# Kernel tuning notes

Hardware: AMD Instinct MI355X
Metric: run time of the kernel (lower is better)

The kernel has to match this reference:

```python
import jax, jax.numpy as jnp
import numpy as np

B, N, DY, STD, T = 2, 8000, 12, 6, 30
DX = 0.5
DYG = 0.5
DT = 1.0

def _mlp(x, params):
    n = len(params)
    for i, (W, b) in enumerate(params):
        x = x @ W + b
        if i < n - 1:
            x = jax.nn.relu(x)
    return x

def _process_param(D, mu, coeff_vec):
    ds = DY // 3
    d33 = ds * ds
    m33 = [coeff_vec[i * d33:(i + 1) * d33].reshape(ds, ds) for i in range(4)]
    base = 4 * d33
    dd = ds * ds - ds
    diag = []
    for i in range(3):
        aij = coeff_vec[base + i * dd:base + (i + 1) * dd].reshape(ds - 1, ds)
        m = jnp.concatenate([jnp.ones((ds - 1, 1), aij.dtype), aij], axis=1).reshape(-1)
        m = jnp.concatenate([m, jnp.ones((1,), aij.dtype)]).reshape(ds, ds)
        diag.append(m)
    z = jnp.zeros((ds, ds), coeff_vec.dtype)
    rows = jnp.concatenate([
        jnp.concatenate([diag[0], z, m33[0]], axis=1),
        jnp.concatenate([z, diag[1], m33[1]], axis=1),
        jnp.concatenate([m33[2], m33[3], diag[2]], axis=1)], axis=0)
    coeffM = jax.nn.relu(rows)  # [DY, DY]
    ds0 = jnp.zeros((ds,), D.dtype)
    Dij = jax.nn.relu(jnp.concatenate([ds0, D]))  # [DY]
    MUij = jax.nn.relu(jnp.concatenate([mu[:ds], ds0, mu[-ds:]]))  # [DY]
    return coeffM, Dij, MUij

def _overlap(t, g):
    # overlap length of unit intervals centered at t and g
    omin = jax.nn.relu((t - 0.5) - (g - 0.5)) + (g - 0.5)
    omax = (t + 0.5) - jax.nn.relu((t + 0.5) - (g + 0.5))
    return jax.nn.relu(omax - omin)

def _trans_probs(dx_, dy_):
    gx, gy = jnp.meshgrid(jnp.arange(5.0), jnp.arange(5.0), indexing='ij')
    grid = jnp.stack([gx, gy], -1).reshape(25, 2)
    xl = _overlap(dx_[..., None, :], grid[:, 1].reshape(1, 1, 25, 1))
    yl = _overlap(dy_[..., None, :], grid[:, 0].reshape(1, 1, 25, 1))
    return xl * yl  # [B,N,25,C]

def _aggre(inp, a0):
    x = inp[:, a0]  # [B,N,25,C] gather
    w = jnp.concatenate([jnp.ones((1,)), jnp.full((24,), 0.01)]).reshape(1, 1, 25, 1)
    return jnp.concatenate([inp, (x * w).sum(-2)], axis=-1)

def _pde(phi, feat_dy, feat_st, D, mu, coeff_vec, trans_p, q_p, dec_p, adj4, adj25, ckpt=False):
    a4 = adj4[0]   # [N,4]
    a0 = adj25[0]  # [N,25]
    coeffM, Dij, MUij = _process_param(D, mu, coeff_vec)
    phie = phi[..., None]
    pn = phie[:, a4]  # [B,N,4,1]
    gpx = (pn[:, :, 1] - pn[:, :, 0]) / (2 * DX)
    gpy = (pn[:, :, 3] - pn[:, :, 2]) / (2 * DYG)
    phi_ag = _aggre(phie, a0)      # constant across steps
    st_ag = _aggre(feat_st, a0)    # constant across steps
    D_bn = jnp.broadcast_to(jax.lax.stop_gradient(Dij), (B, N, DY))
    MU_bn = jnp.broadcast_to(jax.lax.stop_gradient(MUij), (B, N, DY))

    def step(feat, _):
        last = feat
        fn = feat[:, a4]  # [B,N,4,C]
        J = (fn[:, :, 0] + fn[:, :, 1] - 2 * feat) / DX ** 2 + (fn[:, :, 2] + fn[:, :, 3] - 2 * feat) / DYG ** 2
        fxn = (gpx * feat)[:, a4]
        fyn = (gpy * feat)[:, a4]
        Fdiv = (fxn[:, :, 1] - fxn[:, :, 0]) / (2 * DX) + (fyn[:, :, 3] - fyn[:, :, 2]) / (2 * DYG)
        u_diff = jnp.einsum('bnc,cd->bnd', Dij * J - MUij * Fdiv, coeffM)
        mass = jnp.where(last == 0, 1.0, last)
        a_x = jnp.clip(jnp.einsum('bnc,cd->bnd', MUij * gpx, coeffM) / mass, -2.0, 2.0)
        a_y = jnp.clip(jnp.einsum('bnc,cd->bnd', MUij * gpy, coeffM) / mass, -2.0, 2.0)
        probs = _trans_probs(a_x * DT, a_y * DT)  # [B,N,25,C]
        src = probs * last[:, :, None, :]
        scat = lambda idx, s: jnp.zeros((N, DY), s.dtype).at[idx.reshape(-1)].add(s.reshape(-1, DY))
        u_rig = jax.vmap(scat)(adj25, src) - last  # scatter_add over nodes then sum over 25
        feat_tr = jnp.concatenate([_aggre(feat, a0), phi_ag, D_bn, MU_bn, st_ag], -1)  # [B,N,62]
        mix = jax.nn.sigmoid(_mlp(feat_tr, trans_p)[..., -1:])
        delta_u = mix * u_diff + (1 - mix) * u_rig
        feat_q = jnp.concatenate([_aggre(last, a0), phi_ag, st_ag], -1)  # [B,N,38]
        q0 = _mlp(feat_q, q_p)
        new = last + delta_u + q0
        fu = _mlp(jnp.concatenate([new, feat_st], -1), dec_p)  # [B,N,1]
        return new, (fu[..., 0], mix[..., 0], q0, new)

    body = jax.checkpoint(step) if ckpt else step
    _, (us_s, mix_s, q0_s, fd_s) = jax.lax.scan(body, feat_dy, None, length=T)
    us = jnp.moveaxis(us_s, 0, -1).reshape(B, N, 1, T)
    mix_m = jnp.moveaxis(mix_s, 0, -1).reshape(B, N, 1, T)
    q0_m = jnp.moveaxis(q0_s, 0, -1).reshape(B, N, DY, 1, T)
    fd = jnp.moveaxis(fd_s, 0, 2).reshape(B, N, 1, T, DY)
    return us, mix_m, q0_m, fd

def setup_inputs():
    key = jax.random.key(0)
    ks = jax.random.split(key, 24)
    def lin(k, i, o):
        kw, kb = jax.random.split(k)
        return (0.1 * jax.random.normal(kw, (i, o), jnp.float32),
                0.01 * jax.random.normal(kb, (o,), jnp.float32))
    tp = [lin(ks[0], 62, 64), lin(ks[1], 64, 32), lin(ks[2], 32, 26)]
    qp = [lin(ks[3], 38, 64), lin(ks[4], 64, 32), lin(ks[5], 32, 12)]
    dp = [lin(ks[6], 18, 32), lin(ks[7], 32, 32), lin(ks[8], 32, 64), lin(ks[9], 64, 1)]
    inp = {
        'phi': jax.random.normal(ks[10], (B, N), jnp.float32),
        'feat_dy': jax.random.uniform(ks[11], (B, N, DY), jnp.float32),
        'feat_st': jax.random.normal(ks[12], (B, N, STD), jnp.float32),
        'D': jnp.ones((2 * (DY // 3),), jnp.float32) * 0.05,
        'mu': jnp.ones((2 * (DY // 3),), jnp.float32) * 0.05,
        'coeff_vec': jnp.ones((DY * DY - 2 * (DY // 3) ** 2 - DY,), jnp.float32) * 0.05,
        'adj4': jax.random.randint(ks[13], (B, N, 4), 0, N),
        'adj25': jax.random.randint(ks[14], (B, N, 25), 0, N),
    }
    for name, p in [('trans', tp), ('q', qp), ('dec', dp)]:
        for i, (W, b) in enumerate(p):
            inp[name + '_W' + str(i)] = W
            inp[name + '_b' + str(i)] = b
    return inp

def reference(phi, feat_dy, feat_st, D, mu, coeff_vec,
              trans_W0, trans_b0, trans_W1, trans_b1, trans_W2, trans_b2,
              q_W0, q_b0, q_W1, q_b1, q_W2, q_b2,
              dec_W0, dec_b0, dec_W1, dec_b1, dec_W2, dec_b2, dec_W3, dec_b3,
              adj4, adj25):
    trans_p = [(trans_W0, trans_b0), (trans_W1, trans_b1), (trans_W2, trans_b2)]
    q_p = [(q_W0, q_b0), (q_W1, q_b1), (q_W2, q_b2)]
    dec_p = [(dec_W0, dec_b0), (dec_W1, dec_b1), (dec_W2, dec_b2), (dec_W3, dec_b3)]
    return _pde(phi, feat_dy, feat_st, D, mu, coeff_vec, trans_p, q_p, dec_p, adj4, adj25)
```

## Files before the change

### kernel.cpp

```cpp
#include <hip/hip_runtime.h>
#include <hip/hip_fp16.h>
#include <math.h>


namespace {
constexpr int NB = 2;
constexpr int NN = 8000;
constexpr int BN = NB * NN;
constexpr int TS = 30;
constexpr int CAP = 64;

constexpr int P_T0 = 0;
constexpr int P_Q0 = 1536;
constexpr int P_W1 = 3072;
constexpr int P_Q2 = 7168;
constexpr int P_Z  = 7552;
constexpr int P_D0 = 7584;
constexpr int P_D1 = 7968;
constexpr int P_D2 = 8992;
constexpr int P_D3 = 11040;
constexpr int P_BT1 = 11104;
constexpr int P_BQ1 = 11136;
constexpr int P_BQ2 = 11168;
constexpr int P_BD1 = 11184;
constexpr int P_BD2 = 11216;
constexpr int P_MISC= 11280;
constexpr int PACK_N = 11296;

constexpr int A_AG = 0;
constexpr int A_NV = 0;
constexpr int A_H1 = 24;
constexpr int A_D1 = 24;
constexpr int A_D2 = 56;
constexpr int A_H2 = 152;
constexpr int A_SLOT = 216;

constexpr int O_COEFF = 0;
constexpr int O_CFT   = 144;
constexpr int O_DIJ   = 288;
constexpr int O_MUIJ  = 300;
constexpr int O_MC    = 312;
constexpr int O_PACK  = 336;
constexpr int O_GPX   = O_PACK + PACK_N + 16;
constexpr int O_GPY   = O_GPX + BN;
constexpr int O_H1T   = O_GPY + BN;
constexpr int O_H1Q   = O_H1T + BN*64;
constexpr int O_H1D   = O_H1Q + BN*64;
constexpr int O_FEATA = O_H1D + BN*32;
constexpr int O_FEATB = O_FEATA + BN*12;
constexpr int O_AXY2A = O_FEATB + BN*12;
constexpr int O_AXY2B = O_AXY2A + BN*24;
constexpr int O_ACT   = O_AXY2B + BN*24;
constexpr int O_FLTEND= O_ACT + BN*48;
constexpr int O_STG   = O_FLTEND + BN + BN*CAP;
constexpr int STG_N = TS*BN*12;
constexpr size_t WS_NEED = (size_t)(O_STG + STG_N) * 4;

constexpr int OUS  = 0;
constexpr int OMIX = BN*TS;
constexpr int OQ0  = 2*BN*TS;
constexpr int OFD  = OQ0 + BN*12*TS;
}

__device__ __forceinline__ float group5_sum(float v, int lane) {
  int g = lane / 12, c = lane % 12;
  float s1 = __shfl(v, c + 12*((g+1)%5));
  float s2 = __shfl(v, c + 12*((g+2)%5));
  float s3 = __shfl(v, c + 12*((g+3)%5));
  float s4 = __shfl(v, c + 12*((g+4)%5));
  return v + s1 + s2 + s3 + s4;
}

__device__ __forceinline__ float pack_axy(float a, float b) {
  union { __half2 h2; float f; } cv;
  cv.h2 = __floats2half2_rn(a, b);
  return cv.f;
}
__device__ __forceinline__ void unpack_axy(float p, float& a, float& b) {
  union { float f; __half2 h2; } cv;
  cv.f = p;
  a = __low2float(cv.h2);
  b = __high2float(cv.h2);
}

__global__ void k_setup_small(const float* __restrict__ D, const float* __restrict__ mu,
                              const float* __restrict__ cv, float* ws) {
  int t = threadIdx.x;
  for (int e = t; e < 144; e += 256) {
    int r = e / 12, q = e % 12;
    int rb = r >> 2, cb = q >> 2, ri = r & 3, qi = q & 3;
    float val = 0.f;
    if (rb == cb) {
      int f = ri*4 + qi;
      if (f % 5 == 0) val = 1.f;
      else val = cv[64 + rb*12 + (f/5)*4 + (f%5) - 1];
    } else if (rb == 0 && cb == 2) val = cv[     ri*4 + qi];
    else if   (rb == 1 && cb == 2) val = cv[16 + ri*4 + qi];
    else if   (rb == 2 && cb == 0) val = cv[32 + ri*4 + qi];
    else if   (rb == 2 && cb == 1) val = cv[48 + ri*4 + qi];
    ws[O_COEFF + e] = fmaxf(val, 0.f);
  }
  if (t < 12) {
    ws[O_DIJ + t]  = (t < 4) ? 0.f : fmaxf(D[t-4], 0.f);
    ws[O_MUIJ + t] = (t < 4) ? fmaxf(mu[t], 0.f) : ((t < 8) ? 0.f : fmaxf(mu[t-4], 0.f));
  }
  __syncthreads();
  if (t < 144) {
    int r = t / 12, c = t % 12;
    ws[O_CFT + c*12 + r] = ws[O_COEFF + t];
  }
  if (t < 12) {
    float acc = 0.f;
    for (int c = 0; c < 12; c++) acc += ws[O_MUIJ + c] * ws[O_COEFF + c*12 + t];
    ws[O_MC + t] = acc;
  }
}

__global__ void k_xpose(const float* __restrict__ Wt0, const float* __restrict__ Wq0,
                        const float* __restrict__ Wt1, const float* __restrict__ Wq1,
                        const float* __restrict__ Wt2, const float* __restrict__ Wq2,
                        const float* __restrict__ Wd0, const float* __restrict__ Wd1,
                        const float* __restrict__ Wd2, const float* __restrict__ Wd3,
                        const float* __restrict__ bt1, const float* __restrict__ bq1,
                        const float* __restrict__ bt2, const float* __restrict__ bq2,
                        const float* __restrict__ bd1, const float* __restrict__ bd2,
                        const float* __restrict__ bd3,
                        float* ws) {
  const int t = blockIdx.x * blockDim.x + threadIdx.x;
  const int G = gridDim.x * blockDim.x;
  float* P = ws + O_PACK;
  for (int e = t; e < 1536; e += G) {
    int q = e / 256, r = e % 256, l = r / 4, j = r % 4;
    P[P_T0 + e] = Wt0[(4*q+j)*64 + l];
    P[P_Q0 + e] = Wq0[(4*q+j)*64 + l];
  }
  for (int e = t; e < 4096; e += G) {
    int q = e / 256, r = e % 256, l = r / 4, j = r % 4;
    P[P_W1 + e] = (l < 32) ? Wt1[(4*q+j)*32 + l] : Wq1[(4*q+j)*32 + (l-32)];
  }
  for (int e = t; e < 384; e += G) {
    int q = e / 48, r = e % 48, c = r / 4, j = r % 4;
    P[P_Q2 + e] = Wq2[(4*q+j)*12 + c];
  }
  for (int e = t; e < 32; e += G) P[P_Z + e] = Wt2[e*26 + 25];
  for (int e = t; e < 384; e += G) {
    int q = e / 128, r = e % 128, l = r / 4, j = r % 4;
    P[P_D0 + e] = Wd0[(4*q+j)*32 + l];
  }
  for (int e = t; e < 1024; e += G) {
    int q = e / 128, r = e % 128, l = r / 4, j = r % 4;
    P[P_D1 + e] = Wd1[(4*q+j)*32 + l];
  }
  for (int e = t; e < 2048; e += G) {
    int q = e / 256, r = e % 256, l = r / 4, j = r % 4;
    P[P_D2 + e] = Wd2[(4*q+j)*64 + l];
  }
  for (int e = t; e < 64; e += G) P[P_D3 + e] = Wd3[e];
  for (int e = t; e < 32; e += G) {
    P[P_BT1 + e] = bt1[e];
    P[P_BQ1 + e] = bq1[e];
    P[P_BD1 + e] = bd1[e];
  }
  for (int e = t; e < 12; e += G) P[P_BQ2 + e] = bq2[e];
  for (int e = t; e < 64; e += G) P[P_BD2 + e] = bd2[e];
  if (t == 0) { P[P_MISC + 0] = bd3[0]; P[P_MISC + 1] = bt2[25]; }
}

__global__ __launch_bounds__(256) void k_setup_node(
    const float* __restrict__ phi, const float* __restrict__ feat_dy,
    const float* __restrict__ feat_st,
    const int* __restrict__ adj4, const int* __restrict__ adj25,
    const float* __restrict__ Wt0, const float* __restrict__ bt0,
    const float* __restrict__ Wq0, const float* __restrict__ bq0,
    const float* __restrict__ Wd0, const float* __restrict__ bd0,
    float* ws, int* wsi) {
  const int wid  = (blockIdx.x * blockDim.x + threadIdx.x) >> 6;
  const int lane = threadIdx.x & 63;
  if (wid >= BN) return;
  const int b = wid / NN, n = wid % NN;

  const int* a4 = adj4 + n*4;
  const float gpx = phi[b*NN + a4[1]] - phi[b*NN + a4[0]];
  const float gpy = phi[b*NN + a4[3]] - phi[b*NN + a4[2]];
  if (lane == 0) { ws[O_GPX + wid] = gpx; ws[O_GPY + wid] = gpy; wsi[wid] = 0; }

  int idx = 0; float w = 0.f;
  if (lane < 25) { idx = adj25[n*25 + lane]; w = (lane == 0) ? 1.f : 0.01f; }
  float phiw = (lane < 25) ? w * phi[b*NN + idx] : 0.f;
  #pragma unroll
  for (int s = 32; s > 0; s >>= 1) phiw += __shfl_xor(phiw, s);

  float stv[6], stw[6];
  #pragma unroll
  for (int j = 0; j < 6; j++) {
    float x = (lane < 25) ? w * feat_st[(b*NN + idx)*6 + j] : 0.f;
    #pragma unroll
    for (int s = 32; s > 0; s >>= 1) x += __shfl_xor(x, s);
    stw[j] = x;
    stv[j] = feat_st[(b*NN + n)*6 + j];
  }
  const float phiv = phi[b*NN + n];

  float hT = bt0[lane] + phiv*Wt0[24*64 + lane] + phiw*Wt0[25*64 + lane];
  float hQ = bq0[lane] + phiv*Wq0[24*64 + lane] + phiw*Wq0[25*64 + lane];
  #pragma unroll
  for (int i = 0; i < 12; i++) {
    hT = fmaf(ws[O_DIJ  + i], Wt0[(26+i)*64 + lane], hT);
    hT = fmaf(ws[O_MUIJ + i], Wt0[(38+i)*64 + lane], hT);
  }
  #pragma unroll
  for (int j = 0; j < 6; j++) {
    hT = fmaf(stv[j], Wt0[(50+j)*64 + lane], hT);
    hT = fmaf(stw[j], Wt0[(56+j)*64 + lane], hT);
    hQ = fmaf(stv[j], Wq0[(26+j)*64 + lane], hQ);
    hQ = fmaf(stw[j], Wq0[(32+j)*64 + lane], hQ);
  }
  ws[O_H1T + wid*64 + lane] = hT;
  ws[O_H1Q + wid*64 + lane] = hQ;
  if (lane < 32) {
    float hD = bd0[lane];
    #pragma unroll
    for (int j = 0; j < 6; j++) hD = fmaf(stv[j], Wd0[(12+j)*32 + lane], hD);
    ws[O_H1D + wid*32 + lane] = hD;
  }
  if (lane < 12) {
    float f = feat_dy[wid*12 + lane];
    ws[O_FEATA + wid*12 + lane] = f;
    float mass = (f == 0.f) ? 1.f : f;
    float mc = ws[O_MC + lane];
    float axv = fminf(fmaxf(gpx*mc/mass, -2.f), 2.f);
    float ayv = fminf(fmaxf(gpy*mc/mass, -2.f), 2.f);
    float2* a2a = (float2*)(ws + O_AXY2A);
    a2a[wid*12 + lane] = make_float2(f, pack_axy(axv, ayv));
  }
}

__global__ void k_build_rev(const int* __restrict__ adj25, int* wsi) {
  int i = blockIdx.x * blockDim.x + threadIdx.x;
  if (i >= BN * 25) return;
  int b = i / (NN * 25);
  int rem = i % (NN * 25);
  int m = rem / 25, k = rem % 25;
  int tgt = adj25[i];
  int slot = atomicAdd(&wsi[b*NN + tgt], 1);
  if (slot < CAP) wsi[BN + (b*NN + tgt)*CAP + slot] = (m << 5) | k;
}

__global__ __launch_bounds__(512) void k_gather(
    const float* __restrict__ ws,
    const int* __restrict__ rcnt, const int* __restrict__ rent,
    const float* __restrict__ fsrc, const float2* __restrict__ a2src,
    const int* __restrict__ adj4, const int* __restrict__ adj25,
    float* __restrict__ actb) {
  const int wid_raw = (int)((blockIdx.x * blockDim.x + threadIdx.x) >> 6);
  if (wid_raw >= BN) return;
  const int wid  = __builtin_amdgcn_readfirstlane(wid_raw);
  const int lane = threadIdx.x & 63;
  const int c12  = lane % 12;
  const int g    = lane / 12;
  const int b = wid / NN, n = wid % NN;

  const int* a4p = adj4 + n*4;
  const int m0 = a4p[0], m1 = a4p[1], m2 = a4p[2], m3 = a4p[3];
  int cnt = rcnt[wid]; if (cnt > CAP) cnt = CAP;
  const int idxv = (lane < 25) ? adj25[n*25 + lane] : 0;
  const int pkv  = rent[wid*CAP + lane];
  const float f_c  = fsrc[wid*12 + c12];
  const float dij  = ws[O_DIJ  + c12];
  const float muij = ws[O_MUIJ + c12];
  const float4* CFTp = (const float4*)(ws + O_CFT + c12*12);
  const float4 cf0 = CFTp[0], cf1 = CFTp[1], cf2 = CFTp[2];

  float agw = 0.f;
  {
    const int i0 = __shfl(idxv, g);
    const int i1 = __shfl(idxv, g + 5);
    const int i2 = __shfl(idxv, g + 10);
    const int i3 = __shfl(idxv, g + 15);
    const int i4 = __shfl(idxv, g + 20);
    if (g < 5) {
      const float v0 = fsrc[(b*NN + i0)*12 + c12];
      const float v1 = fsrc[(b*NN + i1)*12 + c12];
      const float v2 = fsrc[(b*NN + i2)*12 + c12];
      const float v3 = fsrc[(b*NN + i3)*12 + c12];
      const float v4 = fsrc[(b*NN + i4)*12 + c12];
      const float w0 = (g == 0) ? 1.f : 0.01f;
      agw = fmaf(w0,    v0, agw);
      agw = fmaf(0.01f, v1, agw);
      agw = fmaf(0.01f, v2, agw);
      agw = fmaf(0.01f, v3, agw);
      agw = fmaf(0.01f, v4, agw);
    }
    agw = group5_sum(agw, lane);
  }

  float udiff;
  {
    const float f0 = fsrc[(b*NN+m0)*12 + c12];
    const float f1 = fsrc[(b*NN+m1)*12 + c12];
    const float f2 = fsrc[(b*NN+m2)*12 + c12];
    const float f3 = fsrc[(b*NN+m3)*12 + c12];
    const float gx0 = ws[O_GPX + b*NN + m0], gx1 = ws[O_GPX + b*NN + m1];
    const float gy2 = ws[O_GPY + b*NN + m2], gy3 = ws[O_GPY + b*NN + m3];
    const float J = 4.f * ((f0+f1+f2+f3) - 4.f*f_c);
    const float Fdiv = gx1*f1 - gx0*f0 + gy3*f3 - gy2*f2;
    const float v = dij*J - muij*Fdiv;
    float acc;
    acc  = __shfl(v, 0) * cf0.x;
    acc  = fmaf(__shfl(v, 1), cf0.y, acc);
    acc  = fmaf(__shfl(v, 2), cf0.z, acc);
    acc  = fmaf(__shfl(v, 3), cf0.w, acc);
    acc  = fmaf(__shfl(v, 4), cf1.x, acc);
    acc  = fmaf(__shfl(v, 5), cf1.y, acc);
    acc  = fmaf(__shfl(v, 6), cf1.z, acc);
    acc  = fmaf(__shfl(v, 7), cf1.w, acc);
    acc  = fmaf(__shfl(v, 8), cf2.x, acc);
    acc  = fmaf(__shfl(v, 9), cf2.y, acc);
    acc  = fmaf(__shfl(v,10), cf2.z, acc);
    acc  = fmaf(__shfl(v,11), cf2.w, acc);
    udiff = acc;
  }

  float urig;
  {
    float usc = 0.f;
    #pragma unroll
    for (int it = 0; it < 8; ++it) {
      const int e = g + 5*it;
      const bool val = (g < 5) && (e < cnt);
      const int pk = __shfl(pkv, e & 63);
      const int m = pk >> 5, k = pk & 31;
      const int off = val ? ((b*NN + m)*12 + c12) : (wid*12 + c12);
      const float2 sm = a2src[off];
      float ax, ay; unpack_axy(sm.y, ax, ay);
      const float kx = (float)(k - (k/5)*5);
      const float ky = (float)(k/5);
      const float px = fmaxf(1.f - fabsf(ax - kx), 0.f);
      const float py = fmaxf(1.f - fabsf(ay - ky), 0.f);
      usc = fmaf(val ? px*py : 0.f, sm.x, usc);
    }
    if (cnt > 40) {
      #pragma unroll
      for (int it = 8; it < 13; ++it) {
        const int e = g + 5*it;
        const bool val = (g < 5) && (e < cnt);
        const int pk = __shfl(pkv, e & 63);
        const int m = pk >> 5, k = pk & 31;
        const int off = val ? ((b*NN + m)*12 + c12) : (wid*12 + c12);
        const float2 sm = a2src[off];
        float ax, ay; unpack_axy(sm.y, ax, ay);
        const float kx = (float)(k - (k/5)*5);
        const float ky = (float)(k/5);
        const float px = fmaxf(1.f - fabsf(ax - kx), 0.f);
        const float py = fmaxf(1.f - fabsf(ay - ky), 0.f);
        usc = fmaf(val ? px*py : 0.f, sm.x, usc);
      }
    }
    usc = group5_sum(usc, lane);
    urig = usc - f_c;
  }

  const float ov = (lane < 12) ? agw : ((lane < 24) ? udiff : urig);
  if (lane < 36) actb[wid*48 + lane] = ov;
}

__global__ __launch_bounds__(512) void k_mlp(
    const float* __restrict__ ws, const float* __restrict__ actb, int t,
    const float* __restrict__ fsrc,
    float* __restrict__ fdst, float2* __restrict__ a2dst,
    float* __restrict__ stg, int use_stage,
    float* __restrict__ out) {
  __shared__ __attribute__((aligned(16))) float sh[PACK_N + 16*A_SLOT];
  const int tid = threadIdx.x;
  {
    const float4* wp = (const float4*)(ws + O_PACK);
    float4* sp = (float4*)sh;
    for (int e = tid; e < PACK_N/4; e += 512) sp[e] = wp[e];
  }
  __syncthreads();

  const int wv   = tid >> 6;
  const int wvq  = __builtin_amdgcn_readfirstlane(wv);
  const int lane = tid & 63;
  const int c12 = lane % 12;
  const int l32 = lane & 31;
  const bool isQ = lane >= 32;
  float* act0 = sh + PACK_N + (wvq*2 + 0)*A_SLOT;
  float* act1 = sh + PACK_N + (wvq*2 + 1)*A_SLOT;

  const float mcv = ws[O_MC + c12];

  #pragma unroll 1
  for (int pass = 0; pass < 2; pass++) {
    const int nb = (blockIdx.x*16 + pass*8 + wvq) * 2;

    float f_c[2], udiff[2], urig[2];
    #pragma unroll
    for (int j = 0; j < 2; j++) {
      const int wid = nb + j;
      float* actj = j ? act1 : act0;
      f_c[j] = fsrc[wid*12 + c12];
      const float agv = actb[wid*48 + c12];
      udiff[j] = actb[wid*48 + 12 + c12];
      urig[j]  = actb[wid*48 + 24 + c12];
      if (lane < 24) actj[A_AG + lane] = (lane < 12) ? f_c[j] : agv;
    }

    {
      float h1t0 = ws[O_H1T + nb*64 + lane];
      float h1q0 = ws[O_H1Q + nb*64 + lane];
      float h1t1 = ws[O_H1T + (nb+1)*64 + lane];
      float h1q1 = ws[O_H1Q + (nb+1)*64 + lane];
      #pragma unroll
      for (int q = 0; q < 6; q++) {
        const float4 wt = *(const float4*)&sh[P_T0 + q*256 + lane*4];
        const float4 wq = *(const float4*)&sh[P_Q0 + q*256 + lane*4];
        const float4 a0 = *(const float4*)&act0[A_AG + 4*q];
        const float4 a1 = *(const float4*)&act1[A_AG + 4*q];
        h1t0 = fmaf(a0.x, wt.x, h1t0); h1q0 = fmaf(a0.x, wq.x, h1q0);
        h1t0 = fmaf(a0.y, wt.y, h1t0); h1q0 = fmaf(a0.y, wq.y, h1q0);
        h1t0 = fmaf(a0.z, wt.z, h1t0); h1q0 = fmaf(a0.z, wq.z, h1q0);
        h1t0 = fmaf(a0.w, wt.w, h1t0); h1q0 = fmaf(a0.w, wq.w, h1q0);
        h1t1 = fmaf(a1.x, wt.x, h1t1); h1q1 = fmaf(a1.x, wq.x, h1q1);
        h1t1 = fmaf(a1.y, wt.y, h1t1); h1q1 = fmaf(a1.y, wq.y, h1q1);
        h1t1 = fmaf(a1.z, wt.z, h1t1); h1q1 = fmaf(a1.z, wq.z, h1q1);
        h1t1 = fmaf(a1.w, wt.w, h1t1); h1q1 = fmaf(a1.w, wq.w, h1q1);
      }
      act0[A_H1 + lane]      = fmaxf(h1t0, 0.f);
      act0[A_H1 + 64 + lane] = fmaxf(h1q0, 0.f);
      act1[A_H1 + lane]      = fmaxf(h1t1, 0.f);
      act1[A_H1 + 64 + lane] = fmaxf(h1q1, 0.f);
    }

    {
      const int hoff = isQ ? 64 : 0;
      float h2_0 = isQ ? sh[P_BQ1 + l32] : sh[P_BT1 + l32];
      float h2_1 = h2_0;
      #pragma unroll
      for (int q = 0; q < 16; q++) {
        const float4 w  = *(const float4*)&sh[P_W1 + q*256 + lane*4];
        const float4 a0 = *(const float4*)&act0[A_H1 + hoff + 4*q];
        const float4 a1 = *(const float4*)&act1[A_H1 + hoff + 4*q];
        h2_0 = fmaf(a0.x, w.x, h2_0); h2_1 = fmaf(a1.x, w.x, h2_1);
        h2_0 = fmaf(a0.y, w.y, h2_0); h2_1 = fmaf(a1.y, w.y, h2_1);
        h2_0 = fmaf(a0.z, w.z, h2_0); h2_1 = fmaf(a1.z, w.z, h2_1);
        h2_0 = fmaf(a0.w, w.w, h2_0); h2_1 = fmaf(a1.w, w.w, h2_1);
      }
      act0[A_H2 + lane] = fmaxf(h2_0, 0.f);
      act1[A_H2 + lane] = fmaxf(h2_1, 0.f);
    }

    float mix[2], q0v[2];
    {
      float mz0 = sh[P_MISC + 1], mz1 = mz0;
      float q00 = sh[P_BQ2 + c12], q01 = q00;
      #pragma unroll
      for (int q = 0; q < 8; q++) {
        const float4 wz  = *(const float4*)&sh[P_Z + 4*q];
        const float4 wq  = *(const float4*)&sh[P_Q2 + q*48 + c12*4];
        const float4 at0 = *(const float4*)&act0[A_H2 + 4*q];
        const float4 aq0 = *(const float4*)&act0[A_H2 + 32 + 4*q];
        const float4 at1 = *(const float4*)&act1[A_H2 + 4*q];
        const float4 aq1 = *(const float4*)&act1[A_H2 + 32 + 4*q];
        mz0 = fmaf(at0.x, wz.x, mz0); q00 = fmaf(aq0.x, wq.x, q00);
        mz0 = fmaf(at0.y, wz.y, mz0); q00 = fmaf(aq0.y, wq.y, q00);
        mz0 = fmaf(at0.z, wz.z, mz0); q00 = fmaf(aq0.z, wq.z, q00);
        mz0 = fmaf(at0.w, wz.w, mz0); q00 = fmaf(aq0.w, wq.w, q00);
        mz1 = fmaf(at1.x, wz.x, mz1); q01 = fmaf(aq1.x, wq.x, q01);
        mz1 = fmaf(at1.y, wz.y, mz1); q01 = fmaf(aq1.y, wq.y, q01);
        mz1 = fmaf(at1.z, wz.z, mz1); q01 = fmaf(aq1.z, wq.z, q01);
        mz1 = fmaf(at1.w, wz.w, mz1); q01 = fmaf(aq1.w, wq.w, q01);
      }
      mix[0] = 1.f / (1.f + expf(-mz0));
      mix[1] = 1.f / (1.f + expf(-mz1));
      q0v[0] = q00; q0v[1] = q01;
    }

    #pragma unroll
    for (int j = 0; j < 2; j++) {
      const int wid = nb + j;
      float* actj = j ? act1 : act0;
      const float newv = f_c[j] + mix[j]*udiff[j] + (1.f - mix[j])*urig[j] + q0v[j];
      if (lane < 12) {
        actj[A_NV + lane] = newv;
        if (use_stage) stg[(size_t)t*BN*12 + wid*12 + lane] = q0v[j];
        else           out[OQ0 + (wid*12 + lane)*TS + t] = q0v[j];
        out[OFD + (wid*TS + t)*12 + lane] = newv;
        fdst[wid*12 + lane] = newv;
        float mass = (newv == 0.f) ? 1.f : newv;
        float gpxn = ws[O_GPX + wid], gpyn = ws[O_GPY + wid];
        float axn = fminf(fmaxf(gpxn*mcv/mass, -2.f), 2.f);
        float ayn = fminf(fmaxf(gpyn*mcv/mass, -2.f), 2.f);
        a2dst[wid*12 + lane] = make_float2(newv, pack_axy(axn, ayn));
      }
      if (lane == 0) out[OMIX + wid*TS + t] = mix[j];
    }

    {
      float d1_0 = ws[O_H1D + nb*32 + l32];
      float d1_1 = ws[O_H1D + (nb+1)*32 + l32];
      #pragma unroll
      for (int q = 0; q < 3; q++) {
        const float4 w  = *(const float4*)&sh[P_D0 + q*128 + l32*4];
        const float4 a0 = *(const float4*)&act0[A_NV + 4*q];
        const float4 a1 = *(const float4*)&act1[A_NV + 4*q];
        d1_0 = fmaf(a0.x, w.x, d1_0); d1_1 = fmaf(a1.x, w.x, d1_1);
        d1_0 = fmaf(a0.y, w.y, d1_0); d1_1 = fmaf(a1.y, w.y, d1_1);
        d1_0 = fmaf(a0.z, w.z, d1_0); d1_1 = fmaf(a1.z, w.z, d1_1);
        d1_0 = fmaf(a0.w, w.w, d1_0); d1_1 = fmaf(a1.w, w.w, d1_1);
      }
      if (lane < 32) {
        act0[A_D1 + lane] = fmaxf(d1_0, 0.f);
        act1[A_D1 + lane] = fmaxf(d1_1, 0.f);
      }
    }
    {
      float d2_0 = sh[P_BD1 + l32], d2_1 = d2_0;
      #pragma unroll
      for (int q = 0; q < 8; q++) {
        const float4 w  = *(const float4*)&sh[P_D1 + q*128 + l32*4];
        const float4 a0 = *(const float4*)&act0[A_D1 + 4*q];
        const float4 a1 = *(const float4*)&act1[A_D1 + 4*q];
        d2_0 = fmaf(a0.x, w.x, d2_0); d2_1 = fmaf(a1.x, w.x, d2_1);
        d2_0 = fmaf(a0.y, w.y, d2_0); d2_1 = fmaf(a1.y, w.y, d2_1);
        d2_0 = fmaf(a0.z, w.z, d2_0); d2_1 = fmaf(a1.z, w.z, d2_1);
        d2_0 = fmaf(a0.w, w.w, d2_0); d2_1 = fmaf(a1.w, w.w, d2_1);
      }
      if (lane < 32) {
        act0[A_D2 + lane] = fmaxf(d2_0, 0.f);
        act1[A_D2 + lane] = fmaxf(d2_1, 0.f);
      }
    }
    {
      float d3_0 = sh[P_BD2 + lane], d3_1 = d3_0;
      #pragma unroll
      for (int q = 0; q < 8; q++) {
        const float4 w  = *(const float4*)&sh[P_D2 + q*256 + lane*4];
        const float4 a0 = *(const float4*)&act0[A_D2 + 4*q];
        const float4 a1 = *(const float4*)&act1[A_D2 + 4*q];
        d3_0 = fmaf(a0.x, w.x, d3_0); d3_1 = fmaf(a1.x, w.x, d3_1);
        d3_0 = fmaf(a0.y, w.y, d3_0); d3_1 = fmaf(a1.y, w.y, d3_1);
        d3_0 = fmaf(a0.z, w.z, d3_0); d3_1 = fmaf(a1.z, w.z, d3_1);
        d3_0 = fmaf(a0.w, w.w, d3_0); d3_1 = fmaf(a1.w, w.w, d3_1);
      }
      const float wd3 = sh[P_D3 + lane];
      float u0 = fmaxf(d3_0, 0.f) * wd3;
      float u1 = fmaxf(d3_1, 0.f) * wd3;
      #pragma unroll
      for (int s2 = 32; s2 > 0; s2 >>= 1) {
        u0 += __shfl_xor(u0, s2);
        u1 += __shfl_xor(u1, s2);
      }
      if (lane == 0) {
        const float b3 = sh[P_MISC + 0];
        out[OUS + nb*TS + t]     = u0 + b3;
        out[OUS + (nb+1)*TS + t] = u1 + b3;
      }
    }
  }
}

__global__ void k_out(const float* __restrict__ stg, float* __restrict__ out) {
  const size_t NQ = (size_t)BN*12*TS;
  size_t i = (size_t)blockIdx.x * blockDim.x + threadIdx.x;
  if (i < NQ) {
    int e = (int)(i / TS), t = (int)(i % TS);
    out[OQ0 + i] = stg[(size_t)t*BN*12 + e];
  }
}

extern "C" void kernel_launch(void* const* d_in, const int* in_sizes, int n_in,
                              void* d_out, int out_size, void* d_ws, size_t ws_size,
                              hipStream_t stream) {
  const float* phi     = (const float*)d_in[0];
  const float* feat_dy = (const float*)d_in[1];
  const float* feat_st = (const float*)d_in[2];
  const float* Dv      = (const float*)d_in[3];
  const float* muv     = (const float*)d_in[4];
  const float* cv      = (const float*)d_in[5];
  const int*   adj4    = (const int*)d_in[6];
  const int*   adj25   = (const int*)d_in[7];
  const float* Wt0 = (const float*)d_in[8];
  const float* bt0 = (const float*)d_in[9];
  const float* Wt1 = (const float*)d_in[10];
  const float* bt1 = (const float*)d_in[11];
  const float* Wt2 = (const float*)d_in[12];
  const float* bt2 = (const float*)d_in[13];
  const float* Wq0 = (const float*)d_in[14];
  const float* bq0 = (const float*)d_in[15];
  const float* Wq1 = (const float*)d_in[16];
  const float* bq1 = (const float*)d_in[17];
  const float* Wq2 = (const float*)d_in[18];
  const float* bq2 = (const float*)d_in[19];
  const float* Wd0 = (const float*)d_in[20];
  const float* bd0 = (const float*)d_in[21];
  const float* Wd1 = (const float*)d_in[22];
  const float* bd1 = (const float*)d_in[23];
  const float* Wd2 = (const float*)d_in[24];
  const float* bd2 = (const float*)d_in[25];
  const float* Wd3 = (const float*)d_in[26];
  const float* bd3 = (const float*)d_in[27];

  float* ws  = (float*)d_ws;
  int*   wsi = (int*)(ws + O_FLTEND);
  float* out = (float*)d_out;
  const int use_stage = (ws_size >= WS_NEED) ? 1 : 0;
  float* stg = ws + O_STG;
  float* actb = ws + O_ACT;

  k_setup_small<<<1, 256, 0, stream>>>(Dv, muv, cv, ws);
  k_xpose<<<16, 256, 0, stream>>>(Wt0, Wq0, Wt1, Wq1, Wt2, Wq2, Wd0, Wd1, Wd2, Wd3,
                                  bt1, bq1, bt2, bq2, bd1, bd2, bd3, ws);
  k_setup_node<<<BN/4, 256, 0, stream>>>(phi, feat_dy, feat_st, adj4, adj25,
                                         Wt0, bt0, Wq0, bq0, Wd0, bd0, ws, wsi);
  k_build_rev<<<(BN*25 + 255)/256, 256, 0, stream>>>(adj25, wsi);

  float* fa = ws + O_FEATA; float* fb = ws + O_FEATB;
  float2* pa = (float2*)(ws + O_AXY2A);
  float2* pb = (float2*)(ws + O_AXY2B);
  for (int t = 0; t < TS; t++) {
    k_gather<<<BN/8, 512, 0, stream>>>(ws, wsi, wsi + BN, fa, pa, adj4, adj25, actb);
    k_mlp<<<BN/32, 512, 0, stream>>>(ws, actb, t, fa, fb, pb, stg, use_stage, out);
    float* tf = fa; fa = fb; fb = tf;
    float2* tp = pa; pa = pb; pb = tp;
  }
  if (use_stage) {
    const size_t tot = (size_t)BN*12*TS;
    k_out<<<(unsigned)((tot + 255)/256), 256, 0, stream>>>(stg, out);
  }
}
```

Before: 1.239 ms.

## Fuse gather and MLP kernels into one per-timestep kernel via shared memory

Result: slower. 1.284 ms (+3.6%).

```diff
diff --git a/kernel.cpp b/kernel.cpp
--- a/kernel.cpp
+++ b/kernel.cpp
@@ -35,6 +35,10 @@
 constexpr int A_H2 = 152;
 constexpr int A_SLOT = 216;
 
+constexpr int G_SLOT = 48;
+constexpr int G_ACT  = PACK_N + 16*A_SLOT;
+constexpr int SH_N   = G_ACT + 32*G_SLOT;
+
 constexpr int O_COEFF = 0;
 constexpr int O_CFT   = 144;
 constexpr int O_DIJ   = 288;
@@ -50,8 +54,7 @@
 constexpr int O_FEATB = O_FEATA + BN*12;
 constexpr int O_AXY2A = O_FEATB + BN*12;
 constexpr int O_AXY2B = O_AXY2A + BN*24;
-constexpr int O_ACT   = O_AXY2B + BN*24;
-constexpr int O_FLTEND= O_ACT + BN*48;
+constexpr int O_FLTEND= O_AXY2B + BN*24;
 constexpr int O_STG   = O_FLTEND + BN + BN*CAP;
 constexpr int STG_N = TS*BN*12;
 constexpr size_t WS_NEED = (size_t)(O_STG + STG_N) * 4;
@@ -246,163 +249,163 @@
   if (slot < CAP) wsi[BN + (b*NN + tgt)*CAP + slot] = (m << 5) | k;
 }
 
-__global__ __launch_bounds__(512) void k_gather(
+__global__ __launch_bounds__(512) void k_step3(
     const float* __restrict__ ws,
-    const int* __restrict__ rcnt, const int* __restrict__ rent,
+    const int* __restrict__ rcnt, const int* __restrict__ rent, int t,
     const float* __restrict__ fsrc, const float2* __restrict__ a2src,
+    float* __restrict__ fdst, float2* __restrict__ a2dst,
     const int* __restrict__ adj4, const int* __restrict__ adj25,
-    float* __restrict__ actb) {
-  const int wid_raw = (int)((blockIdx.x * blockDim.x + threadIdx.x) >> 6);
-  if (wid_raw >= BN) return;
-  const int wid  = __builtin_amdgcn_readfirstlane(wid_raw);
-  const int lane = threadIdx.x & 63;
-  const int c12  = lane % 12;
-  const int g    = lane / 12;
-  const int b = wid / NN, n = wid % NN;
-
-  const int* a4p = adj4 + n*4;
-  const int m0 = a4p[0], m1 = a4p[1], m2 = a4p[2], m3 = a4p[3];
-  int cnt = rcnt[wid]; if (cnt > CAP) cnt = CAP;
-  const int idxv = (lane < 25) ? adj25[n*25 + lane] : 0;
-  const int pkv  = rent[wid*CAP + lane];
-  const float f_c  = fsrc[wid*12 + c12];
-  const float dij  = ws[O_DIJ  + c12];
-  const float muij = ws[O_MUIJ + c12];
-  const float4* CFTp = (const float4*)(ws + O_CFT + c12*12);
-  const float4 cf0 = CFTp[0], cf1 = CFTp[1], cf2 = CFTp[2];
-
-  float agw = 0.f;
-  {
-    const int i0 = __shfl(idxv, g);
-    const int i1 = __shfl(idxv, g + 5);
-    const int i2 = __shfl(idxv, g + 10);
-    const int i3 = __shfl(idxv, g + 15);
-    const int i4 = __shfl(idxv, g + 20);
-    if (g < 5) {
-      const float v0 = fsrc[(b*NN + i0)*12 + c12];
-      const float v1 = fsrc[(b*NN + i1)*12 + c12];
-      const float v2 = fsrc[(b*NN + i2)*12 + c12];
-      const float v3 = fsrc[(b*NN + i3)*12 + c12];
-      const float v4 = fsrc[(b*NN + i4)*12 + c12];
-      const float w0 = (g == 0) ? 1.f : 0.01f;
-      agw = fmaf(w0,    v0, agw);
-      agw = fmaf(0.01f, v1, agw);
-      agw = fmaf(0.01f, v2, agw);
-      agw = fmaf(0.01f, v3, agw);
-      agw = fmaf(0.01f, v4, agw);
-    }
-    agw = group5_sum(agw, lane);
-  }
-
-  float udiff;
-  {
-    const float f0 = fsrc[(b*NN+m0)*12 + c12];
-    const float f1 = fsrc[(b*NN+m1)*12 + c12];
-    const float f2 = fsrc[(b*NN+m2)*12 + c12];
-    const float f3 = fsrc[(b*NN+m3)*12 + c12];
-    const float gx0 = ws[O_GPX + b*NN + m0], gx1 = ws[O_GPX + b*NN + m1];
-    const float gy2 = ws[O_GPY + b*NN + m2], gy3 = ws[O_GPY + b*NN + m3];
-    const float J = 4.f * ((f0+f1+f2+f3) - 4.f*f_c);
-    const float Fdiv = gx1*f1 - gx0*f0 + gy3*f3 - gy2*f2;
-    const float v = dij*J - muij*Fdiv;
-    float acc;
-    acc  = __shfl(v, 0) * cf0.x;
-    acc  = fmaf(__shfl(v, 1), cf0.y, acc);
-    acc  = fmaf(__shfl(v, 2), cf0.z, acc);
-    acc  = fmaf(__shfl(v, 3), cf0.w, acc);
-    acc  = fmaf(__shfl(v, 4), cf1.x, acc);
-    acc  = fmaf(__shfl(v, 5), cf1.y, acc);
-    acc  = fmaf(__shfl(v, 6), cf1.z, acc);
-    acc  = fmaf(__shfl(v, 7), cf1.w, acc);
-    acc  = fmaf(__shfl(v, 8), cf2.x, acc);
-    acc  = fmaf(__shfl(v, 9), cf2.y, acc);
-    acc  = fmaf(__shfl(v,10), cf2.z, acc);
-    acc  = fmaf(__shfl(v,11), cf2.w, acc);
-    udiff = acc;
-  }
-
-  float urig;
-  {
-    float usc = 0.f;
-    #pragma unroll
-    for (int it = 0; it < 8; ++it) {
-      const int e = g + 5*it;
-      const bool val = (g < 5) && (e < cnt);
-      const int pk = __shfl(pkv, e & 63);
-      const int m = pk >> 5, k = pk & 31;
-      const int off = val ? ((b*NN + m)*12 + c12) : (wid*12 + c12);
-      const float2 sm = a2src[off];
-      float ax, ay; unpack_axy(sm.y, ax, ay);
-      const float kx = (float)(k - (k/5)*5);
-      const float ky = (float)(k/5);
-      const float px = fmaxf(1.f - fabsf(ax - kx), 0.f);
-      const float py = fmaxf(1.f - fabsf(ay - ky), 0.f);
-      usc = fmaf(val ? px*py : 0.f, sm.x, usc);
-    }
-    if (cnt > 40) {
-      #pragma unroll
-      for (int it = 8; it < 13; ++it) {
-        const int e = g + 5*it;
-        const bool val = (g < 5) && (e < cnt);
-        const int pk = __shfl(pkv, e & 63);
-        const int m = pk >> 5, k = pk & 31;
-        const int off = val ? ((b*NN + m)*12 + c12) : (wid*12 + c12);
-        const float2 sm = a2src[off];
-        float ax, ay; unpack_axy(sm.y, ax, ay);
-        const float kx = (float)(k - (k/5)*5);
-        const float ky = (float)(k/5);
-        const float px = fmaxf(1.f - fabsf(ax - kx), 0.f);
-        const float py = fmaxf(1.f - fabsf(ay - ky), 0.f);
-        usc = fmaf(val ? px*py : 0.f, sm.x, usc);
-      }
-    }
-    usc = group5_sum(usc, lane);
-    urig = usc - f_c;
-  }
-
-  const float ov = (lane < 12) ? agw : ((lane < 24) ? udiff : urig);
-  if (lane < 36) actb[wid*48 + lane] = ov;
-}
-
-__global__ __launch_bounds__(512) void k_mlp(
-    const float* __restrict__ ws, const float* __restrict__ actb, int t,
-    const float* __restrict__ fsrc,
-    float* __restrict__ fdst, float2* __restrict__ a2dst,
     float* __restrict__ stg, int use_stage,
     float* __restrict__ out) {
-  __shared__ __attribute__((aligned(16))) float sh[PACK_N + 16*A_SLOT];
+  __shared__ __attribute__((aligned(16))) float sh[SH_N];
   const int tid = threadIdx.x;
   {
     const float4* wp = (const float4*)(ws + O_PACK);
     float4* sp = (float4*)sh;
     for (int e = tid; e < PACK_N/4; e += 512) sp[e] = wp[e];
   }
-  __syncthreads();
 
   const int wv   = tid >> 6;
   const int wvq  = __builtin_amdgcn_readfirstlane(wv);
   const int lane = tid & 63;
   const int c12 = lane % 12;
+  const int g   = lane / 12;
   const int l32 = lane & 31;
   const bool isQ = lane >= 32;
+
+  {
+    const int nbase = blockIdx.x*32 + wvq*4;
+    const int b = nbase / NN;
+    const float dij  = ws[O_DIJ  + c12];
+    const float muij = ws[O_MUIJ + c12];
+    const float4* CFTp = (const float4*)(ws + O_CFT + c12*12);
+    const float4 cf0 = CFTp[0], cf1 = CFTp[1], cf2 = CFTp[2];
+
+    #pragma unroll
+    for (int i = 0; i < 4; i++) {
+      const int wid = nbase + i;
+      const int n = wid - b*NN;
+      const int* a4p = adj4 + n*4;
+      const int m0 = a4p[0], m1 = a4p[1], m2 = a4p[2], m3 = a4p[3];
+      int cnt = rcnt[wid]; if (cnt > CAP) cnt = CAP;
+      const int idxv = (lane < 25) ? adj25[n*25 + lane] : 0;
+      const int pkv  = rent[wid*CAP + lane];
+      const float f_c = fsrc[wid*12 + c12];
+
+      float agw = 0.f;
+      {
+        const int i0 = __shfl(idxv, g);
+        const int i1 = __shfl(idxv, g + 5);
+        const int i2 = __shfl(idxv, g + 10);
+        const int i3 = __shfl(idxv, g + 15);
+        const int i4 = __shfl(idxv, g + 20);
+        if (g < 5) {
+          const float v0 = fsrc[(b*NN + i0)*12 + c12];
+          const float v1 = fsrc[(b*NN + i1)*12 + c12];
+          const float v2 = fsrc[(b*NN + i2)*12 + c12];
+          const float v3 = fsrc[(b*NN + i3)*12 + c12];
+          const float v4 = fsrc[(b*NN + i4)*12 + c12];
+          const float w0 = (g == 0) ? 1.f : 0.01f;
+          agw = fmaf(w0,    v0, agw);
+          agw = fmaf(0.01f, v1, agw);
+          agw = fmaf(0.01f, v2, agw);
+          agw = fmaf(0.01f, v3, agw);
+          agw = fmaf(0.01f, v4, agw);
+        }
+        agw = group5_sum(agw, lane);
+      }
+
+      float udiff;
+      {
+        const float f0 = fsrc[(b*NN+m0)*12 + c12];
+        const float f1 = fsrc[(b*NN+m1)*12 + c12];
+        const float f2 = fsrc[(b*NN+m2)*12 + c12];
+        const float f3 = fsrc[(b*NN+m3)*12 + c12];
+        const float gx0 = ws[O_GPX + b*NN + m0], gx1 = ws[O_GPX + b*NN + m1];
+        const float gy2 = ws[O_GPY + b*NN + m2], gy3 = ws[O_GPY + b*NN + m3];
+        const float J = 4.f * ((f0+f1+f2+f3) - 4.f*f_c);
+        const float Fdiv = gx1*f1 - gx0*f0 + gy3*f3 - gy2*f2;
+        const float v = dij*J - muij*Fdiv;
+        float acc;
+        acc  = __shfl(v, 0) * cf0.x;
+        acc  = fmaf(__shfl(v, 1), cf0.y, acc);
+        acc  = fmaf(__shfl(v, 2), cf0.z, acc);
+        acc  = fmaf(__shfl(v, 3), cf0.w, acc);
+        acc  = fmaf(__shfl(v, 4), cf1.x, acc);
+        acc  = fmaf(__shfl(v, 5), cf1.y, acc);
+        acc  = fmaf(__shfl(v, 6), cf1.z, acc);
+        acc  = fmaf(__shfl(v, 7), cf1.w, acc);
+        acc  = fmaf(__shfl(v, 8), cf2.x, acc);
+        acc  = fmaf(__shfl(v, 9), cf2.y, acc);
+        acc  = fmaf(__shfl(v,10), cf2.z, acc);
+        acc  = fmaf(__shfl(v,11), cf2.w, acc);
+        udiff = acc;
+      }
+
+      float urig;
+      {
+        float usc = 0.f;
+        #pragma unroll
+        for (int it = 0; it < 8; ++it) {
+          const int e = g + 5*it;
+          const bool val = (g < 5) && (e < cnt);
+          const int pk = __shfl(pkv, e & 63);
+          const int m = pk >> 5, k = pk & 31;
+          const int off = val ? ((b*NN + m)*12 + c12) : (wid*12 + c12);
+          const float2 sm = a2src[off];
+          float ax, ay; unpack_axy(sm.y, ax, ay);
+          const float kx = (float)(k - (k/5)*5);
+          const float ky = (float)(k/5);
+          const float px = fmaxf(1.f - fabsf(ax - kx), 0.f);
+          const float py = fmaxf(1.f - fabsf(ay - ky), 0.f);
+          usc = fmaf(val ? px*py : 0.f, sm.x, usc);
+        }
+        if (cnt > 40) {
+          #pragma unroll
+          for (int it = 8; it < 13; ++it) {
+            const int e = g + 5*it;
+            const bool val = (g < 5) && (e < cnt);
+            const int pk = __shfl(pkv, e & 63);
+            const int m = pk >> 5, k = pk & 31;
+            const int off = val ? ((b*NN + m)*12 + c12) : (wid*12 + c12);
+            const float2 sm = a2src[off];
+            float ax, ay; unpack_axy(sm.y, ax, ay);
+            const float kx = (float)(k - (k/5)*5);
+            const float ky = (float)(k/5);
+            const float px = fmaxf(1.f - fabsf(ax - kx), 0.f);
+            const float py = fmaxf(1.f - fabsf(ay - ky), 0.f);
+            usc = fmaf(val ? px*py : 0.f, sm.x, usc);
+          }
+        }
+        usc = group5_sum(usc, lane);
+        urig = usc - f_c;
+      }
+
+      const float ov = (lane < 12) ? agw
+                     : ((lane < 24) ? udiff
+                     : ((lane < 36) ? urig : f_c));
+      if (lane < 48) sh[G_ACT + (wvq*4 + i)*G_SLOT + lane] = ov;
+    }
+  }
+  __syncthreads();
+
   float* act0 = sh + PACK_N + (wvq*2 + 0)*A_SLOT;
   float* act1 = sh + PACK_N + (wvq*2 + 1)*A_SLOT;
-
   const float mcv = ws[O_MC + c12];
 
   #pragma unroll 1
   for (int pass = 0; pass < 2; pass++) {
-    const int nb = (blockIdx.x*16 + pass*8 + wvq) * 2;
+    const int lnb = (pass*8 + wvq)*2;
+    const int nb  = blockIdx.x*32 + lnb;
 
     float f_c[2], udiff[2], urig[2];
     #pragma unroll
     for (int j = 0; j < 2; j++) {
-      const int wid = nb + j;
       float* actj = j ? act1 : act0;
-      f_c[j] = fsrc[wid*12 + c12];
-      const float agv = actb[wid*48 + c12];
-      udiff[j] = actb[wid*48 + 12 + c12];
-      urig[j]  = actb[wid*48 + 24 + c12];
+      const float agv = sh[G_ACT + (lnb+j)*G_SLOT + c12];
+      udiff[j] = sh[G_ACT + (lnb+j)*G_SLOT + 12 + c12];
+      urig[j]  = sh[G_ACT + (lnb+j)*G_SLOT + 24 + c12];
+      f_c[j]   = sh[G_ACT + (lnb+j)*G_SLOT + 36 + c12];
       if (lane < 24) actj[A_AG + lane] = (lane < 12) ? f_c[j] : agv;
     }
 
@@ -606,7 +609,6 @@
   float* out = (float*)d_out;
   const int use_stage = (ws_size >= WS_NEED) ? 1 : 0;
   float* stg = ws + O_STG;
-  float* actb = ws + O_ACT;
 
   k_setup_small<<<1, 256, 0, stream>>>(Dv, muv, cv, ws);
   k_xpose<<<16, 256, 0, stream>>>(Wt0, Wq0, Wt1, Wq1, Wt2, Wq2, Wd0, Wd1, Wd2, Wd3,
@@ -619,8 +621,8 @@
   float2* pa = (float2*)(ws + O_AXY2A);
   float2* pb = (float2*)(ws + O_AXY2B);
   for (int t = 0; t < TS; t++) {
-    k_gather<<<BN/8, 512, 0, stream>>>(ws, wsi, wsi + BN, fa, pa, adj4, adj25, actb);
-    k_mlp<<<BN/32, 512, 0, stream>>>(ws, actb, t, fa, fb, pb, stg, use_stage, out);
+    k_step3<<<BN/32, 512, 0, stream>>>(ws, wsi, wsi + BN, t, fa, pa, fb, pb,
+                                       adj4, adj25, stg, use_stage, out);
     float* tf = fa; fa = fb; fb = tf;
     float2* tp = pa; pa = pb; pb = tp;
   }
```
